# Kernel tuning notes

Measured on AMD Instinct MI355X. Metric: run time of the kernel, lower is better.

## Reference

```python
import jax, jax.numpy as jnp
import numpy as np

E = 256

def setup_inputs() -> dict:
    key = jax.random.key(0)
    ks = jax.random.split(key, 10)
    N, T_y, T_x = 8, 300, 160
    s = 1.0 / np.sqrt(E)  # torch-style uniform-ish init scale, keeps gates unsaturated
    return {
        "inputs": jax.random.normal(ks[0], (N, T_y, E // 2), jnp.float32),
        "memory": jax.random.normal(ks[1], (N, T_x, E), jnp.float32),
        "h0": jnp.zeros((1, N, E), jnp.float32),
        "Wih": jax.random.normal(ks[2], (3 * E, E // 2), jnp.float32) * s,
        "Whh": jax.random.normal(ks[3], (3 * E, E), jnp.float32) * s,
        "bih": jax.random.normal(ks[4], (3 * E,), jnp.float32) * s,
        "bhh": jax.random.normal(ks[5], (3 * E,), jnp.float32) * s,
        "W": jax.random.normal(ks[6], (E, E), jnp.float32) * s,
        "U": jax.random.normal(ks[7], (E, E), jnp.float32) * s,
        "v": jax.random.normal(ks[8], (E,), jnp.float32) * s,
    }


def reference(inputs, memory, h0, Wih, Whh, bih, bhh, W, U, v):
    # GRU (PyTorch gate order r, z, n), batch_first, single layer, unidirectional.
    def step(h, x_t):
        gi = x_t @ Wih.T + bih      # [N, 3E]
        gh = h @ Whh.T + bhh        # [N, 3E]
        ir, iz, i_n = jnp.split(gi, 3, axis=-1)
        hr, hz, hn = jnp.split(gh, 3, axis=-1)
        r = jax.nn.sigmoid(ir + hr)
        z = jax.nn.sigmoid(iz + hz)
        n = jnp.tanh(i_n + r * hn)
        h_new = (1.0 - z) * n + z * h
        return h_new, h_new

    h_last, outs = jax.lax.scan(step, h0[0], jnp.swapaxes(inputs, 0, 1))
    outputs = jnp.swapaxes(outs, 0, 1)   # [N, T_y, E]
    hidden = h_last[None]                # [1, N, E]

    # Bahdanau additive attention
    w = outputs @ W.T                    # [N, T_y, E]
    u = memory @ U.T                     # [N, T_x, E]
    # scores: v . tanh(w + u) broadcast over [N, T_y, T_x, E]
    scores = jnp.einsum('ntxe,e->ntx', jnp.tanh(w[:, :, None, :] + u[:, None, :, :]), v)
    attn_weights = jax.nn.softmax(scores, axis=2)  # [N, T_y, T_x]
    return attn_weights, outputs, hidden
```

## Files before the change

kernel.cpp:

```cpp
#include <hip/hip_runtime.h>


typedef _Float16 f16x2 __attribute__((ext_vector_type(2)));
typedef _Float16 f16x8 __attribute__((ext_vector_type(8)));
typedef float f32x4 __attribute__((ext_vector_type(4)));

__device__ __forceinline__ float fexp2(float x) { return __builtin_amdgcn_exp2f(x); }
__device__ __forceinline__ float frcp(float x) { return __builtin_amdgcn_rcpf(x); }
__device__ __forceinline__ float fsig(float x) {
    return frcp(1.0f + fexp2(x * -1.4426950408889634f));
}
__device__ __forceinline__ float ftanh(float x) {
    return 1.0f - 2.0f * frcp(1.0f + fexp2(x * 2.8853900817779268f));
}

__device__ __forceinline__ float pick4(f32x4 v, int s) {
    float ab = (s & 1) ? v[1] : v[0];
    float cd = (s & 1) ? v[3] : v[2];
    return (s & 2) ? cd : ab;
}

#define FLAG(i) ((i) * 32)

__global__ __launch_bounds__(256) void phase1_kernel(
    const float* __restrict__ Whh, unsigned* __restrict__ wd,
    const float* __restrict__ inputs, const float* __restrict__ Wih,
    float* __restrict__ gi, const float* __restrict__ bih,
    const float* __restrict__ bhh, int* flags, int full) {
    if (full && blockIdx.x == 0 && threadIdx.x < 9)
        flags[FLAG(threadIdx.x)] = 0;
    if (blockIdx.x < 384) {
        int gid = blockIdx.x * 256 + threadIdx.x;
        int i = gid >> 9, t = gid & 511;
        int fi = i >> 2, j = i & 3;
        int g = fi >> 4, m2 = (fi >> 3) & 1, ks = fi & 7;
        int w = t >> 6, l = t & 63;
        int row = 256 * g + 32 * w + 16 * m2 + (l & 15);
        int k = 32 * ks + 8 * (l >> 4) + 2 * j;
        union { unsigned u; f16x2 h; } cv;
        cv.h[0] = (_Float16)Whh[(size_t)row * 256 + k];
        cv.h[1] = (_Float16)Whh[(size_t)row * 256 + k + 1];
        wd[i * 512 + t] = cv.u;
        return;
    }
    int id = blockIdx.x - 384;
    const int n0 = (id % 12) * 64, m0 = (id / 12) * 64;
    __shared__ float Xs[32][65];
    __shared__ float Ws2[32][65];
    const int tid = threadIdx.x;
    const int tx = tid & 15, ty = tid >> 4;
    const int M = 2400, K = 128;
    float acc[4][4] = {};
    for (int k0 = 0; k0 < K; k0 += 32) {
#pragma unroll
        for (int i = 0; i < 8; ++i) {
            int e = tid + i * 256;
            int kk = e & 31, m = e >> 5;
            int row = m0 + m;
            Xs[kk][m] = (row < M) ? inputs[(size_t)row * K + k0 + kk] : 0.0f;
            Ws2[kk][m] = Wih[(size_t)(n0 + m) * K + k0 + kk];
        }
        __syncthreads();
#pragma unroll
        for (int kk = 0; kk < 32; ++kk) {
            float a[4], b[4];
#pragma unroll
            for (int i = 0; i < 4; ++i) a[i] = Xs[kk][ty * 4 + i];
#pragma unroll
            for (int j = 0; j < 4; ++j) b[j] = Ws2[kk][tx * 4 + j];
#pragma unroll
            for (int i = 0; i < 4; ++i)
#pragma unroll
                for (int j = 0; j < 4; ++j) acc[i][j] += a[i] * b[j];
        }
        __syncthreads();
    }
#pragma unroll
    for (int i = 0; i < 4; ++i) {
        int row = m0 + ty * 4 + i;
        if (row >= M) continue;
        int b = row / 300;
        int t = row - b * 300;
#pragma unroll
        for (int j = 0; j < 4; ++j) {
            int col = n0 + tx * 4 + j;
            float val = acc[i][j] + ((col < 512) ? (bih[col] + bhh[col]) : bih[col]);
            gi[(size_t)(t * 8 + b) * 768 + col] = val;
        }
    }
}

__global__ __launch_bounds__(256) void gemm_kernel(
    const float* __restrict__ X, const float* __restrict__ Wt,
    float* __restrict__ C, _Float16* __restrict__ C16,
    int M, int N, int K, int mode) {
    __shared__ float Xs[32][65];
    __shared__ float Ws2[32][65];
    const int n0 = blockIdx.x * 64, m0 = blockIdx.y * 64;
    const int tid = threadIdx.x;
    const int tx = tid & 15, ty = tid >> 4;
    float acc[4][4] = {};
    for (int k0 = 0; k0 < K; k0 += 32) {
#pragma unroll
        for (int i = 0; i < 8; ++i) {
            int e = tid + i * 256;
            int kk = e & 31, m = e >> 5;
            int row = m0 + m;
            Xs[kk][m] = (row < M) ? X[(size_t)row * K + k0 + kk] : 0.0f;
            Ws2[kk][m] = Wt[(size_t)(n0 + m) * K + k0 + kk];
        }
        __syncthreads();
#pragma unroll
        for (int kk = 0; kk < 32; ++kk) {
            float a[4], b[4];
#pragma unroll
            for (int i = 0; i < 4; ++i) a[i] = Xs[kk][ty * 4 + i];
#pragma unroll
            for (int j = 0; j < 4; ++j) b[j] = Ws2[kk][tx * 4 + j];
#pragma unroll
            for (int i = 0; i < 4; ++i)
#pragma unroll
                for (int j = 0; j < 4; ++j) acc[i][j] += a[i] * b[j];
        }
        __syncthreads();
    }
#pragma unroll
    for (int i = 0; i < 4; ++i) {
        int row = m0 + ty * 4 + i;
        if (row >= M) continue;
#pragma unroll
        for (int j = 0; j < 4; ++j) {
            int col = n0 + tx * 4 + j;
            if (mode == 2) C16[(size_t)row * N + col] = (_Float16)acc[i][j];
            else           C[(size_t)row * N + col] = acc[i][j];
        }
    }
}

__global__ __launch_bounds__(512, 1) void gru_mega(
    const float* __restrict__ gi, const unsigned* __restrict__ wd,
    const float* __restrict__ h0, const float* __restrict__ bhh,
    float* __restrict__ outs, float* __restrict__ hid,
    const float* __restrict__ memory, const float* __restrict__ Um,
    _Float16* __restrict__ u16, const float* __restrict__ W,
    const float* __restrict__ vv, float* __restrict__ attn,
    int* flags, int full) {
    __shared__ __align__(16) _Float16 hbuf[2][256];
    __shared__ float Xs[32][65];
    __shared__ float Ws2[32][65];
    __shared__ unsigned uS[160 * 129];
    __shared__ __align__(16) float oL[10][260];
    __shared__ float wLf[10][256];
    __shared__ float vL[256];
    __shared__ float scP[2][2][160];
    __shared__ float sc2[2][160];
    __shared__ float red2[2][2];

    const int tid = threadIdx.x;

    if (blockIdx.x >= 8) {
        int id = blockIdx.x - 8;
        if (id < 80) {
            const int n0 = (id & 3) * 64, m0 = (id >> 2) * 64;
            const int tx = tid & 15, ty = (tid & 255) >> 4;
            float acc[4][4] = {};
            for (int k0 = 0; k0 < 256; k0 += 32) {
                if (tid < 256) {
#pragma unroll
                    for (int i = 0; i < 8; ++i) {
                        int e = tid + i * 256;
                        int kk = e & 31, m = e >> 5;
                        Xs[kk][m] = memory[(size_t)(m0 + m) * 256 + k0 + kk];
                        Ws2[kk][m] = Um[(size_t)(n0 + m) * 256 + k0 + kk];
                    }
                }
                __syncthreads();
                if (tid < 256) {
#pragma unroll
                    for (int kk = 0; kk < 32; ++kk) {
                        float a[4], b[4];
#pragma unroll
                        for (int i = 0; i < 4; ++i) a[i] = Xs[kk][ty * 4 + i];
#pragma unroll
                        for (int j = 0; j < 4; ++j) b[j] = Ws2[kk][tx * 4 + j];
#pragma unroll
                        for (int i = 0; i < 4; ++i)
#pragma unroll
                            for (int j = 0; j < 4; ++j) acc[i][j] += a[i] * b[j];
                    }
                }
                __syncthreads();
            }
            if (tid < 256) {
#pragma unroll
                for (int i = 0; i < 4; ++i)
#pragma unroll
                    for (int j = 0; j < 4; ++j)
                        u16[(size_t)(m0 + ty * 4 + i) * 256 + n0 + tx * 4 + j] =
                            (_Float16)acc[i][j];
            }
            if (!full) return;
            __syncthreads();
            if (tid == 0)
                __hip_atomic_fetch_add(&flags[FLAG(8)], 1, __ATOMIC_RELEASE,
                                       __HIP_MEMORY_SCOPE_AGENT);
        }
        if (!full) return;

        const int grp = id / 30;
        const int tc = id % 30;
        if (tid == 0) {
            while (__hip_atomic_load(&flags[FLAG(8)], __ATOMIC_RELAXED,
                                     __HIP_MEMORY_SCOPE_AGENT) < 80)
                __builtin_amdgcn_s_sleep(64);
            while (__hip_atomic_load(&flags[FLAG(8)], __ATOMIC_ACQUIRE,
                                     __HIP_MEMORY_SCOPE_AGENT) < 80)
                __builtin_amdgcn_s_sleep(8);
        }
        __syncthreads();
        const unsigned* ug = (const unsigned*)(u16 + (size_t)grp * 160 * 256);
        for (int i = tid; i < 20480; i += 512)
            uS[(i >> 7) * 129 + (i & 127)] = ug[i];
        if (tid < 256) vL[tid] = vv[tid];
        __syncthreads();

        if (tid == 0) {
            while (__hip_atomic_load(&flags[FLAG(grp)], __ATOMIC_RELAXED,
                                     __HIP_MEMORY_SCOPE_AGENT) < 1)
                __builtin_amdgcn_s_sleep(127);
            while (__hip_atomic_load(&flags[FLAG(grp)], __ATOMIC_ACQUIRE,
                                     __HIP_MEMORY_SCOPE_AGENT) < 1)
                __builtin_amdgcn_s_sleep(8);
        }
        __syncthreads();
        for (int i = tid; i < 2560; i += 512) {
            int ti = i >> 8, k = i & 255;
            oL[ti][k] = outs[((size_t)grp * 300 + tc * 10 + ti) * 256 + k];
        }
        __syncthreads();
        {
            const int c = tid & 255, rh = tid >> 8;
            float a0 = 0, a1 = 0, a2 = 0, a3 = 0, a4 = 0;
            const float* wr = W + (size_t)c * 256;
            const int r0 = rh * 5;
            for (int k4 = 0; k4 < 256; k4 += 4) {
                float4 wq = *(const float4*)(wr + k4);
#define WROW(ACC, TI)                                                     \
                {                                                         \
                    float4 oq = *(const float4*)(&oL[TI][k4]);            \
                    ACC += wq.x * oq.x + wq.y * oq.y +                    \
                           wq.z * oq.z + wq.w * oq.w;                     \
                }
                WROW(a0, r0 + 0) WROW(a1, r0 + 1) WROW(a2, r0 + 2)
                WROW(a3, r0 + 3) WROW(a4, r0 + 4)
#undef WROW
            }
            wLf[r0 + 0][c] = a0; wLf[r0 + 1][c] = a1; wLf[r0 + 2][c] = a2;
            wLf[r0 + 3][c] = a3; wLf[r0 + 4][c] = a4;
        }
        __syncthreads();
        for (int tp = 0; tp < 5; ++tp) {
            const int ti0 = tp * 2;
            if (tid < 320) {
                const int x = (tid < 160) ? tid : tid - 160;
                const int half = (tid >= 160) ? 1 : 0;
                const unsigned* ur = uS + x * 129 + half * 64;
                const float* wl0 = wLf[ti0] + half * 128;
                const float* wl1 = wLf[ti0 + 1] + half * 128;
                const float* vl = vL + half * 128;
                float a0 = 0.f, b0 = 0.f, a1 = 0.f, b1 = 0.f;
#pragma unroll 8
                for (int e2 = 0; e2 < 64; ++e2) {
                    union { unsigned uu2; _Float16 hh[2]; } cv;
                    cv.uu2 = ur[e2];
                    int ee = e2 * 2;
                    float u0 = (float)cv.hh[0], u1 = (float)cv.hh[1];
                    float v0 = vl[ee], v1 = vl[ee + 1];
                    a0 += v0 * ftanh(wl0[ee] + u0);
                    b0 += v1 * ftanh(wl0[ee + 1] + u1);
                    a1 += v0 * ftanh(wl1[ee] + u0);
                    b1 += v1 * ftanh(wl1[ee + 1] + u1);
                }
                scP[0][half][x] = a0 + b0;
                scP[1][half][x] = a1 + b1;
            }
            __syncthreads();
            if (tid < 320) {
                int r = (tid >= 160) ? 1 : 0;
                int x = r ? tid - 160 : tid;
                sc2[r][x] = scP[r][0][x] + scP[r][1][x];
            }
            __syncthreads();
            if (tid < 128) {
                int r = tid >> 6, lane = tid & 63;
                float m = -3.0e38f;
                for (int i = lane; i < 160; i += 64) m = fmaxf(m, sc2[r][i]);
#pragma unroll
                for (int o = 32; o; o >>= 1) m = fmaxf(m, __shfl_xor(m, o));
                if (lane == 0) red2[r][0] = m;
            }
            __syncthreads();
            if (tid < 320) {
                int r = (tid >= 160) ? 1 : 0;
                int x = r ? tid - 160 : tid;
                sc2[r][x] = fexp2((sc2[r][x] - red2[r][0]) *
                                  1.4426950408889634f);
            }
            __syncthreads();
            if (tid < 128) {
                int r = tid >> 6, lane = tid & 63;
                float s = 0.0f;
                for (int i = lane; i < 160; i += 64) s += sc2[r][i];
#pragma unroll
                for (int o = 32; o; o >>= 1) s += __shfl_xor(s, o);
                if (lane == 0) red2[r][1] = s;
            }
            __syncthreads();
            if (tid < 320) {
                int r = (tid >= 160) ? 1 : 0;
                int x = r ? tid - 160 : tid;
                attn[(size_t)(grp * 300 + tc * 10 + ti0 + r) * 160 + x] =
                    sc2[r][x] * frcp(red2[r][1]);
            }
            __syncthreads();
        }
        return;
    }

    const int b = blockIdx.x;
    const int t = tid;
    const int w = t >> 6, l = t & 63;
    const int grp = l >> 4;
    const int sel = l & 7;
    const int hi = (l >> 3) & 1;
    const int m2s = sel >> 2, rsel = sel & 3;
    const int e = 32 * w + 16 * m2s + 4 * grp + rsel;

    f16x8 wf[48];
#pragma unroll
    for (int fi = 0; fi < 48; ++fi) {
        union { unsigned u[4]; f16x8 v; } cv;
#pragma unroll
        for (int j = 0; j < 4; ++j) cv.u[j] = wd[(fi * 4 + j) * 512 + t];
        wf[fi] = cv.v;
    }

    float h = h0[b * 256 + e];
    float bn = bhh[512 + e];
    if (!hi) hbuf[0][e] = (_Float16)h;
    const float* gp = gi + b * 768;
    float* op = outs + (size_t)b * 76800 + e;

    float gr = gp[e], gz = gp[e + 256], gn = gp[e + 512];
    __syncthreads();

    for (int st = 0; st < 300; ++st) {
        int stn = (st < 299) ? st + 1 : st;
        const float* g = gp + (size_t)stn * 6144;
        float grn = g[e], gzn = g[e + 256], gnn = g[e + 512];

        const _Float16* hb = hbuf[st & 1];
        f16x8 hv0 = *(const f16x8*)(hb + 0 * 32 + 8 * grp);
        f16x8 hv1 = *(const f16x8*)(hb + 1 * 32 + 8 * grp);
        f16x8 hv2 = *(const f16x8*)(hb + 2 * 32 + 8 * grp);
        f16x8 hv3 = *(const f16x8*)(hb + 3 * 32 + 8 * grp);
        f16x8 hv4 = *(const f16x8*)(hb + 4 * 32 + 8 * grp);
        f16x8 hv5 = *(const f16x8*)(hb + 5 * 32 + 8 * grp);
        f16x8 hv6 = *(const f16x8*)(hb + 6 * 32 + 8 * grp);
        f16x8 hv7 = *(const f16x8*)(hb + 7 * 32 + 8 * grp);

        f32x4 aR0 = {0.f, 0.f, 0.f, 0.f}, aR1 = {0.f, 0.f, 0.f, 0.f};
        f32x4 aZ0 = {0.f, 0.f, 0.f, 0.f}, aZ1 = {0.f, 0.f, 0.f, 0.f};
        f32x4 aN0 = {0.f, 0.f, 0.f, 0.f}, aN1 = {0.f, 0.f, 0.f, 0.f};
#define KSTEP(ks, hv)                                                        \
        aR0 = __builtin_amdgcn_mfma_f32_16x16x32_f16(wf[0 * 8 + ks], hv, aR0, 0, 0, 0); \
        aR1 = __builtin_amdgcn_mfma_f32_16x16x32_f16(wf[1 * 8 + ks], hv, aR1, 0, 0, 0); \
        aZ0 = __builtin_amdgcn_mfma_f32_16x16x32_f16(wf[2 * 8 + ks], hv, aZ0, 0, 0, 0); \
        aZ1 = __builtin_amdgcn_mfma_f32_16x16x32_f16(wf[3 * 8 + ks], hv, aZ1, 0, 0, 0); \
        aN0 = __builtin_amdgcn_mfma_f32_16x16x32_f16(wf[4 * 8 + ks], hv, aN0, 0, 0, 0); \
        aN1 = __builtin_amdgcn_mfma_f32_16x16x32_f16(wf[5 * 8 + ks], hv, aN1, 0, 0, 0);
        KSTEP(0, hv0) KSTEP(1, hv1) KSTEP(2, hv2) KSTEP(3, hv3)
        KSTEP(4, hv4) KSTEP(5, hv5) KSTEP(6, hv6) KSTEP(7, hv7)
#undef KSTEP

        f32x4 vR = m2s ? aR1 : aR0;
        f32x4 vZ = m2s ? aZ1 : aZ0;
        f32x4 vN = m2s ? aN1 : aN0;
        float sr = pick4(vR, rsel);
        float sz = pick4(vZ, rsel);
        float sn = pick4(vN, rsel);

        float r = fsig(gr + sr);
        float z = fsig(gz + sz);
        float n = ftanh(gn + r * (sn + bn));
        h = n + z * (h - n);

        gr = grn; gz = gzn; gn = gnn;

        if (hi)
            op[st * 256] = h;
        else
            hbuf[(st + 1) & 1][e] = (_Float16)h;
        asm volatile("s_waitcnt lgkmcnt(0)\n\ts_barrier" ::: "memory");
    }
    if (!hi) hid[b * 256 + e] = h;
    if (full) {
        asm volatile("s_waitcnt vmcnt(0)" ::: "memory");
        __syncthreads();
        if (t == 0)
            __hip_atomic_store(&flags[FLAG(b)], 1, __ATOMIC_RELEASE,
                               __HIP_MEMORY_SCOPE_AGENT);
    }
}

__global__ __launch_bounds__(256) void wattn_kernel(
    const _Float16* __restrict__ u16, const float* __restrict__ outs,
    const float* __restrict__ W, const float* __restrict__ vv,
    float* __restrict__ attn) {
    const int tc = blockIdx.x, b = blockIdx.y;
    const int tid = threadIdx.x;
    __shared__ unsigned uS[160 * 129];
    __shared__ __align__(16) float oL[10][260];
    __shared__ float wLf[10][256];
    __shared__ float vL[256], sc[160], red[2];

    const unsigned* ug = (const unsigned*)(u16 + (size_t)b * 160 * 256);
    for (int i = tid; i < 20480; i += 256)
        uS[(i >> 7) * 129 + (i & 127)] = ug[i];
    vL[tid] = vv[tid];
    for (int i = tid; i < 2560; i += 256) {
        int ti = i >> 8, k = i & 255;
        oL[ti][k] = outs[((size_t)b * 300 + tc * 10 + ti) * 256 + k];
    }
    __syncthreads();
    {
        float a0 = 0, a1 = 0, a2 = 0, a3 = 0, a4 = 0;
        float a5 = 0, a6 = 0, a7 = 0, a8 = 0, a9 = 0;
        for (int k4 = 0; k4 < 256; k4 += 4) {
            float4 wq = *(const float4*)(W + (size_t)tid * 256 + k4);
#define WROW(ACC, TI)                                                     \
            {                                                             \
                float4 oq = *(const float4*)(&oL[TI][k4]);                \
                ACC += wq.x * oq.x + wq.y * oq.y +                        \
                       wq.z * oq.z + wq.w * oq.w;                        \
            }
            WROW(a0, 0) WROW(a1, 1) WROW(a2, 2) WROW(a3, 3) WROW(a4, 4)
            WROW(a5, 5) WROW(a6, 6) WROW(a7, 7) WROW(a8, 8) WROW(a9, 9)
#undef WROW
        }
        wLf[0][tid] = a0; wLf[1][tid] = a1; wLf[2][tid] = a2;
        wLf[3][tid] = a3; wLf[4][tid] = a4; wLf[5][tid] = a5;
        wLf[6][tid] = a6; wLf[7][tid] = a7; wLf[8][tid] = a8;
        wLf[9][tid] = a9;
    }
    __syncthreads();
    for (int ti = 0; ti < 10; ++ti) {
        int t = tc * 10 + ti;
        float acc2 = 0.0f;
        if (tid < 160) {
            const unsigned* ur = uS + tid * 129;
            const float* wl = wLf[ti];
#pragma unroll 8
            for (int e2 = 0; e2 < 128; ++e2) {
                union { unsigned uu2; _Float16 hh[2]; } cv;
                cv.uu2 = ur[e2];
                int ee = e2 * 2;
                acc2 += vL[ee] * ftanh(wl[ee] + (float)cv.hh[0]);
                acc2 += vL[ee + 1] * ftanh(wl[ee + 1] + (float)cv.hh[1]);
            }
            sc[tid] = acc2;
        }
        __syncthreads();
        if (tid < 64) {
            float m = -3.0e38f;
            for (int i = tid; i < 160; i += 64) m = fmaxf(m, sc[i]);
#pragma unroll
            for (int o = 32; o; o >>= 1) m = fmaxf(m, __shfl_xor(m, o));
            if (tid == 0) red[0] = m;
        }
        __syncthreads();
        float ee = 0.0f;
        if (tid < 160) {
            ee = fexp2((acc2 - red[0]) * 1.4426950408889634f);
            sc[tid] = ee;
        }
        __syncthreads();
        if (tid < 64) {
            float s = 0.0f;
            for (int i = tid; i < 160; i += 64) s += sc[i];
#pragma unroll
            for (int o = 32; o; o >>= 1) s += __shfl_xor(s, o);
            if (tid == 0) red[1] = s;
        }
        __syncthreads();
        if (tid < 160)
            attn[(size_t)(b * 300 + t) * 160 + tid] = ee * frcp(red[1]);
        __syncthreads();
    }
}

extern "C" void kernel_launch(void* const* d_in, const int* in_sizes, int n_in,
                              void* d_out, int out_size, void* d_ws, size_t ws_size,
                              hipStream_t stream) {
    const float* inputs = (const float*)d_in[0];
    const float* memory = (const float*)d_in[1];
    const float* h0 = (const float*)d_in[2];
    const float* Wih = (const float*)d_in[3];
    const float* Whh = (const float*)d_in[4];
    const float* bih = (const float*)d_in[5];
    const float* bhh = (const float*)d_in[6];
    const float* Wm = (const float*)d_in[7];
    const float* Um = (const float*)d_in[8];
    const float* vv = (const float*)d_in[9];

    float* out = (float*)d_out;
    float* out_attn = out;
    float* out_outputs = out + 384000;
    float* out_hidden = out + 998400;

    char* ws = (char*)d_ws;
    float* gi = (float*)ws;
    unsigned* wd = (unsigned*)(ws + 7372800);

    const size_t U16_OFF = 7766016, FLAG_OFF = 8421376;
    const bool full = ws_size >= FLAG_OFF + 1152;
    _Float16* u16 = full ? (_Float16*)(ws + U16_OFF) : (_Float16*)ws;
    int* flags = (int*)(ws + FLAG_OFF);

    phase1_kernel<<<840, 256, 0, stream>>>(Whh, wd, inputs, Wih, gi, bih, bhh,
                                           flags, full ? 1 : 0);
    if (full) {
        gru_mega<<<248, 512, 0, stream>>>(gi, wd, h0, bhh, out_outputs,
                                          out_hidden, memory, Um, u16, Wm, vv,
                                          out_attn, flags, 1);
    } else {
        gru_mega<<<8, 512, 0, stream>>>(gi, wd, h0, bhh, out_outputs,
                                        out_hidden, memory, Um, u16, Wm, vv,
                                        out_attn, flags, 0);
        gemm_kernel<<<dim3(4, 20), 256, 0, stream>>>(memory, Um, nullptr, u16,
                                                     1280, 256, 256, 2);
        wattn_kernel<<<dim3(30, 8), 256, 0, stream>>>(u16, out_outputs, Wm, vv,
                                                      out_attn);
    }
}
```

Baseline: 450.2 us.

## Fold phase-1 weight repack and input GEMM into the persistent GRU kernel

Moves the Whh fp16 repacking and the input-projection GEMM (inputs·Wih plus biases) out of the separate phase1 launch and into the persistent gru_mega kernel. All 248 blocks stride over the 840 phase-1 tasks, then meet at an atomic-counter grid barrier before the recurrence starts. Flag clearing moves to a hipMemsetAsync. This removes one kernel launch and its inter-kernel gap. In exchange it adds a grid-wide spin barrier, depends on all 248 blocks being co-resident, and uses fewer blocks than before for the phase-1 work.

After: 484.1 us. +7.5%, slower.

```diff
diff --git a/kernel.cpp b/kernel.cpp
--- a/kernel.cpp
+++ b/kernel.cpp
@@ -26,9 +26,7 @@
     const float* __restrict__ Whh, unsigned* __restrict__ wd,
     const float* __restrict__ inputs, const float* __restrict__ Wih,
     float* __restrict__ gi, const float* __restrict__ bih,
-    const float* __restrict__ bhh, int* flags, int full) {
-    if (full && blockIdx.x == 0 && threadIdx.x < 9)
-        flags[FLAG(threadIdx.x)] = 0;
+    const float* __restrict__ bhh) {
     if (blockIdx.x < 384) {
         int gid = blockIdx.x * 256 + threadIdx.x;
         int i = gid >> 9, t = gid & 511;
@@ -138,12 +136,14 @@
 }
 
 __global__ __launch_bounds__(512, 1) void gru_mega(
-    const float* __restrict__ gi, const unsigned* __restrict__ wd,
+    float* __restrict__ gi, unsigned* __restrict__ wd,
     const float* __restrict__ h0, const float* __restrict__ bhh,
     float* __restrict__ outs, float* __restrict__ hid,
     const float* __restrict__ memory, const float* __restrict__ Um,
     _Float16* __restrict__ u16, const float* __restrict__ W,
     const float* __restrict__ vv, float* __restrict__ attn,
+    const float* __restrict__ Whh, const float* __restrict__ inputs,
+    const float* __restrict__ Wih, const float* __restrict__ bih,
     int* flags, int full) {
     __shared__ __align__(16) _Float16 hbuf[2][256];
     __shared__ float Xs[32][65];
@@ -157,6 +157,83 @@
     __shared__ float red2[2][2];
 
     const int tid = threadIdx.x;
+
+    if (full) {
+        for (int task = blockIdx.x; task < 840; task += 248) {
+            if (task < 384) {
+                if (tid < 256) {
+                    int gid = task * 256 + tid;
+                    int i = gid >> 9, t = gid & 511;
+                    int fi = i >> 2, j = i & 3;
+                    int g = fi >> 4, m2 = (fi >> 3) & 1, ks = fi & 7;
+                    int w = t >> 6, l = t & 63;
+                    int row = 256 * g + 32 * w + 16 * m2 + (l & 15);
+                    int k = 32 * ks + 8 * (l >> 4) + 2 * j;
+                    union { unsigned u; f16x2 h; } cv;
+                    cv.h[0] = (_Float16)Whh[(size_t)row * 256 + k];
+                    cv.h[1] = (_Float16)Whh[(size_t)row * 256 + k + 1];
+                    wd[i * 512 + t] = cv.u;
+                }
+            } else {
+                int tt = task - 384;
+                const int n0 = (tt % 12) * 64, m0 = (tt / 12) * 64;
+                const int tx = tid & 15, ty = tid >> 4;
+                float acc[2][4] = {};
+                for (int k0 = 0; k0 < 128; k0 += 32) {
+#pragma unroll
+                    for (int i = 0; i < 4; ++i) {
+                        int e = tid + i * 512;
+                        int kk = e & 31, m = e >> 5;
+                        int row = m0 + m;
+                        Xs[kk][m] = (row < 2400)
+                                        ? inputs[(size_t)row * 128 + k0 + kk]
+                                        : 0.0f;
+                        Ws2[kk][m] = Wih[(size_t)(n0 + m) * 128 + k0 + kk];
+                    }
+                    __syncthreads();
+#pragma unroll
+                    for (int kk = 0; kk < 32; ++kk) {
+                        float a0 = Xs[kk][ty * 2], a1 = Xs[kk][ty * 2 + 1];
+                        float b0 = Ws2[kk][tx * 4 + 0];
+                        float b1 = Ws2[kk][tx * 4 + 1];
+                        float b2 = Ws2[kk][tx * 4 + 2];
+                        float b3 = Ws2[kk][tx * 4 + 3];
+                        acc[0][0] += a0 * b0; acc[0][1] += a0 * b1;
+                        acc[0][2] += a0 * b2; acc[0][3] += a0 * b3;
+                        acc[1][0] += a1 * b0; acc[1][1] += a1 * b1;
+                        acc[1][2] += a1 * b2; acc[1][3] += a1 * b3;
+                    }
+                    __syncthreads();
+                }
+#pragma unroll
+                for (int i = 0; i < 2; ++i) {
+                    int row = m0 + ty * 2 + i;
+                    if (row < 2400) {
+                        int bb = row / 300;
+                        int t2 = row - bb * 300;
+#pragma unroll
+                        for (int j = 0; j < 4; ++j) {
+                            int col = n0 + tx * 4 + j;
+                            float val = acc[i][j] +
+                                ((col < 512) ? (bih[col] + bhh[col]) : bih[col]);
+                            gi[(size_t)(t2 * 8 + bb) * 768 + col] = val;
+                        }
+                    }
+                }
+            }
+            __syncthreads();
+        }
+        asm volatile("s_waitcnt vmcnt(0)" ::: "memory");
+        __syncthreads();
+        if (tid == 0) {
+            __hip_atomic_fetch_add(&flags[FLAG(9)], 1, __ATOMIC_RELEASE,
+                                   __HIP_MEMORY_SCOPE_AGENT);
+            while (__hip_atomic_load(&flags[FLAG(9)], __ATOMIC_ACQUIRE,
+                                     __HIP_MEMORY_SCOPE_AGENT) < 248)
+                __builtin_amdgcn_s_sleep(16);
+        }
+        __syncthreads();
+    }
 
     if (blockIdx.x >= 8) {
         int id = blockIdx.x - 8;
@@ -523,20 +600,23 @@
     unsigned* wd = (unsigned*)(ws + 7372800);
 
     const size_t U16_OFF = 7766016, FLAG_OFF = 8421376;
-    const bool full = ws_size >= FLAG_OFF + 1152;
+    const bool full = ws_size >= FLAG_OFF + 1280;
     _Float16* u16 = full ? (_Float16*)(ws + U16_OFF) : (_Float16*)ws;
     int* flags = (int*)(ws + FLAG_OFF);
 
-    phase1_kernel<<<840, 256, 0, stream>>>(Whh, wd, inputs, Wih, gi, bih, bhh,
-                                           flags, full ? 1 : 0);
     if (full) {
+        hipMemsetAsync(flags, 0, 1280, stream);
         gru_mega<<<248, 512, 0, stream>>>(gi, wd, h0, bhh, out_outputs,
                                           out_hidden, memory, Um, u16, Wm, vv,
-                                          out_attn, flags, 1);
+                                          out_attn, Whh, inputs, Wih, bih,
+                                          flags, 1);
     } else {
+        phase1_kernel<<<840, 256, 0, stream>>>(Whh, wd, inputs, Wih, gi, bih,
+                                               bhh);
         gru_mega<<<8, 512, 0, stream>>>(gi, wd, h0, bhh, out_outputs,
                                         out_hidden, memory, Um, u16, Wm, vv,
-                                        out_attn, flags, 0);
+                                        out_attn, Whh, inputs, Wih, bih,
+                                        flags, 0);
         gemm_kernel<<<dim3(4, 20), 256, 0, stream>>>(memory, Um, nullptr, u16,
                                                      1280, 256, 256, 2);
         wattn_kernel<<<dim3(30, 8), 256, 0, stream>>>(u16, out_outputs, Wm, vv,
```
